# Optimization experiments

Measured on AMD Instinct MI355X. Metric: run time of the kernel, lower is better.

## Reference

```python
import jax, jax.numpy as jnp
import numpy as np

IMG_H = 448
IMG_W = 448
NEG = jnp.float32(-1e30)


def make_anchors(h, w, stride, size):
    # centers at (x*stride, y*stride), single scale, ratio 1; row-major (y, x) order
    ys = jnp.arange(h, dtype=jnp.float32) * stride
    xs = jnp.arange(w, dtype=jnp.float32) * stride
    cy, cx = jnp.meshgrid(ys, xs, indexing='ij')
    cx, cy = cx.reshape(-1), cy.reshape(-1)
    half = 0.5 * size
    return jnp.stack([cx - half, cy - half, cx + half, cy + half], axis=1)  # [h*w, 4]


def iou_one_vs_all(box, boxes):
    x1 = jnp.maximum(box[0], boxes[:, 0]); y1 = jnp.maximum(box[1], boxes[:, 1])
    x2 = jnp.minimum(box[2], boxes[:, 2]); y2 = jnp.minimum(box[3], boxes[:, 3])
    inter = jnp.maximum(x2 - x1, 0.) * jnp.maximum(y2 - y1, 0.)
    a1 = (box[2] - box[0]) * (box[3] - box[1])
    a2 = (boxes[:, 2] - boxes[:, 0]) * (boxes[:, 3] - boxes[:, 1])
    return inter / (a1 + a2 - inter)


def nms_topk(anchors, scores, valid, iou_thr, topk):
    # greedy NMS: invalid (<= mean) boxes get -inf score so they are never selected
    s0 = jnp.where(valid, scores, NEG)

    def body(k, carry):
        s, out = carry
        idx = jnp.argmax(s)
        box = anchors[idx]
        sup = iou_one_vs_all(box, anchors) > iou_thr
        s = jnp.where(sup, NEG, s).at[idx].set(NEG)
        out = out.at[k].set(box)
        return (s, out)

    _, out = jax.lax.fori_loop(0, topk, body, (s0, jnp.zeros((topk, 4), jnp.float32)))
    return out  # [topk, 4]


def get_att_roi(att, stride, size, iou_thr, topk):
    n, _, h, w = att.shape
    corner = jnp.zeros((h, w), att.dtype).at[int(0.1 * h):int(0.9 * h), int(0.1 * w):int(0.9 * w)].set(1.0)
    scores = (att[:, 0] * corner).reshape(n, -1)
    valid = scores > scores.mean(axis=1, keepdims=True)  # score threshold = per-sample mean
    anchors = make_anchors(h, w, float(stride), float(size))
    boxes = jax.vmap(lambda s, v: nms_topk(anchors, s, v, iou_thr, topk))(scores, valid)  # [n, topk, 4]
    boxes = jnp.stack([
        jnp.maximum(boxes[..., 0], 0.),
        jnp.maximum(boxes[..., 1], 0.),
        jnp.minimum(boxes[..., 2], IMG_W - 1.),
        jnp.minimum(boxes[..., 3], IMG_H - 1.),
    ], axis=-1)
    ids = jnp.broadcast_to(jnp.arange(n, dtype=jnp.float32)[:, None, None], (n, topk, 1))
    return jnp.concatenate([ids, boxes], axis=-1).reshape(n * topk, 5)


def crop_resize(xi, x1i, y1i, cw, ch):
    # bilinear resize of integer crop xi[:, y1i:y1i+ch, x1i:x1i+cw] to full (H, W),
    # align_corners=False (matches F.interpolate)
    C, H, W = xi.shape

    def axis_idx(n_out, start, clen):
        s = jnp.maximum((jnp.arange(n_out, dtype=jnp.float32) + 0.5) * (clen.astype(jnp.float32) / n_out) - 0.5, 0.)
        i0 = jnp.floor(s).astype(jnp.int32)
        i1 = jnp.minimum(i0 + 1, clen - 1)
        return start + i0, start + i1, s - i0

    gy0, gy1, fy = axis_idx(H, y1i, ch)
    gx0, gx1, fx = axis_idx(W, x1i, cw)
    x00 = xi[:, gy0[:, None], gx0[None, :]]
    x01 = xi[:, gy0[:, None], gx1[None, :]]
    x10 = xi[:, gy1[:, None], gx0[None, :]]
    x11 = xi[:, gy1[:, None], gx1[None, :]]
    top = x00 + fx[None, None, :] * (x01 - x00)
    bot = x10 + fx[None, None, :] * (x11 - x10)
    return top + fy[None, :, None] * (bot - top)


def forward(x2, x3, x4, x5):
    m3 = x3.mean(1, keepdims=True)
    m4 = x4.mean(1, keepdims=True)
    m5 = x5.mean(1, keepdims=True)
    roi3 = jax.lax.stop_gradient(get_att_roi(m3, 2 ** 3, 64, 0.05, 5))
    roi4 = jax.lax.stop_gradient(get_att_roi(m4, 2 ** 4, 128, 0.05, 3))
    roi5 = jax.lax.stop_gradient(get_att_roi(m5, 2 ** 5, 256, 0.05, 1))
    n = x2.shape[0]
    scale = float(2 ** 3)
    all_b = jnp.concatenate([
        roi3.reshape(n, 5, 5)[..., 1:],
        roi4.reshape(n, 3, 5)[..., 1:],
        roi5.reshape(n, 1, 5)[..., 1:],
    ], axis=1) / scale  # [n, 9, 4] in x2 feature coords
    x1i = jnp.floor(all_b[..., 0].min(1)).astype(jnp.int32)
    y1i = jnp.floor(all_b[..., 1].min(1)).astype(jnp.int32)
    x2i = jnp.floor(all_b[..., 2].max(1)).astype(jnp.int32)
    y2i = jnp.floor(all_b[..., 3].max(1)).astype(jnp.int32)
    crop = jax.vmap(crop_resize)(x2, x1i, y1i, x2i - x1i, y2i - y1i)
    return roi3, roi4, roi5, crop


def setup_inputs() -> dict:
    key = jax.random.key(0)
    k2, k3, k4, k5 = jax.random.split(key, 4)
    return {
        'x2': jax.random.normal(k2, (32, 256, 56, 56), jnp.float32),
        'x3': jax.random.normal(k3, (32, 256, 56, 56), jnp.float32),
        'x4': jax.random.normal(k4, (32, 256, 28, 28), jnp.float32),
        'x5': jax.random.normal(k5, (32, 256, 14, 14), jnp.float32),
    }


def reference(x2, x3, x4, x5):
    return forward(x2, x3, x4, x5)
```

## Files before the change

kernel.cpp:

```cpp
#include <hip/hip_runtime.h>

#define NEGV (-1e30f)

template <int H, int W, int R0, int R1>
__global__ __launch_bounds__(256) void mean_mask_kernel(const float* __restrict__ x,
                                                        float* __restrict__ scores) {
    constexpr int HW = H * W;
    constexpr int QUADS = HW / 4;
    const int tid = threadIdx.x;
    const int cg = tid >> 5;
    const int pl = tid & 31;
    const int q = blockIdx.x * 32 + pl;

    __shared__ float4 part[256];

    float4 acc = make_float4(0.f, 0.f, 0.f, 0.f);
    if (q < 32 * QUADS) {
        const int b = q / QUADS;
        const int quad = q - b * QUADS;
        const float* base = x + (size_t)b * 256 * HW + (size_t)cg * 32 * HW + quad * 4;
#pragma unroll 8
        for (int c = 0; c < 32; ++c) {
            const float4 v = *reinterpret_cast<const float4*>(base + (size_t)c * HW);
            acc.x += v.x; acc.y += v.y; acc.z += v.z; acc.w += v.w;
        }
    }
    part[tid] = acc;
    __syncthreads();

    if (tid < 32 && q < 32 * QUADS) {
        float4 s = part[pl];
#pragma unroll
        for (int g = 1; g < 8; ++g) {
            const float4 v = part[g * 32 + pl];
            s.x += v.x; s.y += v.y; s.z += v.z; s.w += v.w;
        }
        const int b = q / QUADS;
        const int quad = q - b * QUADS;
        const int p0 = quad * 4;
        float r[4] = {s.x, s.y, s.z, s.w};
        float o[4];
#pragma unroll
        for (int e = 0; e < 4; ++e) {
            const int p = p0 + e;
            const int y = p / W;
            const int xx = p - y * W;
            const float val = r[e] * (1.0f / 256.0f);
            const bool in = (y >= R0) && (y < R1) && (xx >= R0) && (xx < R1);
            o[e] = in ? val : 0.0f;
        }
        *reinterpret_cast<float4*>(scores + (size_t)b * HW + p0) =
            make_float4(o[0], o[1], o[2], o[3]);
    }
}

__global__ __launch_bounds__(256) void nms_kernel(const float* __restrict__ sc3,
                                                  const float* __restrict__ sc4,
                                                  const float* __restrict__ sc5,
                                                  float* __restrict__ out) {
    __shared__ float s[3136];
    __shared__ float red_v[256];
    __shared__ int red_i[256];

    const int blk = blockIdx.x;
    const int sid = blk >> 5;
    const int b = blk & 31;

    int HW, Wd, topk;
    float stride, size_;
    const float* sc;
    float* o;
    if (sid == 0) {
        HW = 3136; Wd = 56; topk = 5; stride = 8.f;  size_ = 64.f;
        sc = sc3 + (size_t)b * 3136; o = out + (size_t)(b * 5) * 5;
    } else if (sid == 1) {
        HW = 784;  Wd = 28; topk = 3; stride = 16.f; size_ = 128.f;
        sc = sc4 + (size_t)b * 784;  o = out + 800 + (size_t)(b * 3) * 5;
    } else {
        HW = 196;  Wd = 14; topk = 1; stride = 32.f; size_ = 256.f;
        sc = sc5 + (size_t)b * 196;  o = out + 1280 + (size_t)b * 5;
    }

    const int tid = threadIdx.x;

    float acc = 0.f;
    for (int j = tid; j < HW; j += 256) {
        const float v = sc[j];
        s[j] = v;
        acc += v;
    }
    red_v[tid] = acc;
    __syncthreads();
    for (int off = 128; off > 0; off >>= 1) {
        if (tid < off) red_v[tid] += red_v[tid + off];
        __syncthreads();
    }
    const float mean = red_v[0] / (float)HW;
    __syncthreads();

    for (int j = tid; j < HW; j += 256) {
        const float v = s[j];
        s[j] = (v > mean) ? v : NEGV;
    }
    __syncthreads();

    const float half = 0.5f * size_;
    const float area2 = 2.0f * size_ * size_;

    for (int k = 0; k < topk; ++k) {
        float bv = -3.0e38f;
        int bi = 0x7fffffff;
        for (int j = tid; j < HW; j += 256) {
            const float v = s[j];
            if (v > bv) { bv = v; bi = j; }
        }
        red_v[tid] = bv;
        red_i[tid] = bi;
        __syncthreads();
        for (int off = 128; off > 0; off >>= 1) {
            if (tid < off) {
                const float v2 = red_v[tid + off];
                const int i2 = red_i[tid + off];
                const float v1 = red_v[tid];
                const int i1 = red_i[tid];
                if (v2 > v1 || (v2 == v1 && i2 < i1)) {
                    red_v[tid] = v2;
                    red_i[tid] = i2;
                }
            }
            __syncthreads();
        }
        const int idx = red_i[0];

        const int gy = idx / Wd;
        const int gx = idx - gy * Wd;
        const float cx = (float)gx * stride;
        const float cy = (float)gy * stride;
        const float bx1 = cx - half, by1 = cy - half;
        const float bx2 = cx + half, by2 = cy + half;

        if (tid == 0) {
            float* r = o + (size_t)k * 5;
            r[0] = (float)b;
            r[1] = fmaxf(bx1, 0.f);
            r[2] = fmaxf(by1, 0.f);
            r[3] = fminf(bx2, 447.f);
            r[4] = fminf(by2, 447.f);
        }

        for (int j = tid; j < HW; j += 256) {
            const int ay = j / Wd;
            const int ax = j - ay * Wd;
            const float acx = (float)ax * stride;
            const float acy = (float)ay * stride;
            const float ix1 = fmaxf(bx1, acx - half);
            const float iy1 = fmaxf(by1, acy - half);
            const float ix2 = fminf(bx2, acx + half);
            const float iy2 = fminf(by2, acy + half);
            const float inter = fmaxf(ix2 - ix1, 0.f) * fmaxf(iy2 - iy1, 0.f);
            const float iou = inter / (area2 - inter);
            if (iou > 0.05f || j == idx) s[j] = NEGV;
        }
        __syncthreads();
    }
}

__global__ void bounds_kernel(const float* __restrict__ out, int* __restrict__ bnds) {
    const int b = threadIdx.x;
    if (b >= 32) return;
    float x1 = 3.0e38f, y1 = 3.0e38f, x2 = -3.0e38f, y2 = -3.0e38f;
#pragma unroll
    for (int k = 0; k < 5; ++k) {
        const float* r = out + (size_t)(b * 5 + k) * 5;
        x1 = fminf(x1, r[1]); y1 = fminf(y1, r[2]);
        x2 = fmaxf(x2, r[3]); y2 = fmaxf(y2, r[4]);
    }
#pragma unroll
    for (int k = 0; k < 3; ++k) {
        const float* r = out + 800 + (size_t)(b * 3 + k) * 5;
        x1 = fminf(x1, r[1]); y1 = fminf(y1, r[2]);
        x2 = fmaxf(x2, r[3]); y2 = fmaxf(y2, r[4]);
    }
    {
        const float* r = out + 1280 + (size_t)b * 5;
        x1 = fminf(x1, r[1]); y1 = fminf(y1, r[2]);
        x2 = fmaxf(x2, r[3]); y2 = fmaxf(y2, r[4]);
    }
    const int x1i = (int)floorf(x1 * 0.125f);
    const int y1i = (int)floorf(y1 * 0.125f);
    const int x2i = (int)floorf(x2 * 0.125f);
    const int y2i = (int)floorf(y2 * 0.125f);
    bnds[b * 4 + 0] = x1i;
    bnds[b * 4 + 1] = y1i;
    bnds[b * 4 + 2] = x2i - x1i;
    bnds[b * 4 + 3] = y2i - y1i;
}

__global__ __launch_bounds__(256) void crop_kernel(const float* __restrict__ x2,
                                                   const int* __restrict__ bnds,
                                                   float* __restrict__ out) {
    const int bc = blockIdx.x;
    const int b = bc >> 8;
    const int tid = threadIdx.x;

    const int x1i = bnds[b * 4 + 0];
    const int y1i = bnds[b * 4 + 1];
    const int cw = bnds[b * 4 + 2];
    const int ch = bnds[b * 4 + 3];
    const float sxs = (float)cw / 56.0f;
    const float sys = (float)ch / 56.0f;

    const float* plane = x2 + (size_t)bc * 3136;
    float* op = out + (size_t)bc * 3136;

    for (int p = tid; p < 3136; p += 256) {
        const int y = p / 56;
        const int xx = p - y * 56;
        const float sy = fmaxf((y + 0.5f) * sys - 0.5f, 0.f);
        const float sx = fmaxf((xx + 0.5f) * sxs - 0.5f, 0.f);
        const int iy0 = (int)sy;
        const int ix0 = (int)sx;
        const float fy = sy - (float)iy0;
        const float fx = sx - (float)ix0;
        const int iy1 = min(iy0 + 1, ch - 1);
        const int ix1 = min(ix0 + 1, cw - 1);
        const int gy0 = (y1i + iy0) * 56;
        const int gy1 = (y1i + iy1) * 56;
        const int gx0 = x1i + ix0;
        const int gx1 = x1i + ix1;
        const float v00 = plane[gy0 + gx0];
        const float v01 = plane[gy0 + gx1];
        const float v10 = plane[gy1 + gx0];
        const float v11 = plane[gy1 + gx1];
        const float top = v00 + fx * (v01 - v00);
        const float bot = v10 + fx * (v11 - v10);
        op[p] = top + fy * (bot - top);
    }
}

extern "C" void kernel_launch(void* const* d_in, const int* in_sizes, int n_in,
                              void* d_out, int out_size, void* d_ws, size_t ws_size,
                              hipStream_t stream) {
    const float* x2 = (const float*)d_in[0];
    const float* x3 = (const float*)d_in[1];
    const float* x4 = (const float*)d_in[2];
    const float* x5 = (const float*)d_in[3];
    float* out = (float*)d_out;

    float* sc3 = (float*)d_ws;
    float* sc4 = sc3 + 32 * 3136;
    float* sc5 = sc4 + 32 * 784;
    int* bnds = (int*)(sc5 + 32 * 196);

    mean_mask_kernel<56, 56, 5, 50><<<784, 256, 0, stream>>>(x3, sc3);
    mean_mask_kernel<28, 28, 2, 25><<<196, 256, 0, stream>>>(x4, sc4);
    mean_mask_kernel<14, 14, 1, 12><<<49, 256, 0, stream>>>(x5, sc5);

    nms_kernel<<<96, 256, 0, stream>>>(sc3, sc4, sc5, out);

    bounds_kernel<<<1, 64, 0, stream>>>(out, bnds);

    crop_kernel<<<8192, 256, 0, stream>>>(x2, bnds, out + 1440);
}
```

Baseline: 319.8 us.

## Fuse mean kernels, register-resident NMS, precomputed crop interpolation tables

```diff
diff --git a/kernel.cpp b/kernel.cpp
--- a/kernel.cpp
+++ b/kernel.cpp
@@ -3,40 +3,36 @@
 #define NEGV (-1e30f)
 
 template <int H, int W, int R0, int R1>
-__global__ __launch_bounds__(256) void mean_mask_kernel(const float* __restrict__ x,
-                                                        float* __restrict__ scores) {
+__device__ __forceinline__ void mean_body(int blk, const float* __restrict__ x,
+                                          float* __restrict__ scores,
+                                          float4* part) {
     constexpr int HW = H * W;
     constexpr int QUADS = HW / 4;
     const int tid = threadIdx.x;
     const int cg = tid >> 5;
     const int pl = tid & 31;
-    const int q = blockIdx.x * 32 + pl;
-
-    __shared__ float4 part[256];
+    const int q = blk * 32 + pl;
+
+    const int b = q / QUADS;
+    const int quad = q - b * QUADS;
+    const float* base = x + (size_t)b * 256 * HW + (size_t)cg * 32 * HW + quad * 4;
 
     float4 acc = make_float4(0.f, 0.f, 0.f, 0.f);
-    if (q < 32 * QUADS) {
-        const int b = q / QUADS;
-        const int quad = q - b * QUADS;
-        const float* base = x + (size_t)b * 256 * HW + (size_t)cg * 32 * HW + quad * 4;
 #pragma unroll 8
-        for (int c = 0; c < 32; ++c) {
-            const float4 v = *reinterpret_cast<const float4*>(base + (size_t)c * HW);
-            acc.x += v.x; acc.y += v.y; acc.z += v.z; acc.w += v.w;
-        }
+    for (int c = 0; c < 32; ++c) {
+        const float4 v = *reinterpret_cast<const float4*>(base + (size_t)c * HW);
+        acc.x += v.x; acc.y += v.y; acc.z += v.z; acc.w += v.w;
     }
     part[tid] = acc;
     __syncthreads();
 
-    if (tid < 32 && q < 32 * QUADS) {
+    if (tid < 32) {
         float4 s = part[pl];
 #pragma unroll
         for (int g = 1; g < 8; ++g) {
             const float4 v = part[g * 32 + pl];
             s.x += v.x; s.y += v.y; s.z += v.z; s.w += v.w;
         }
-        const int b = q / QUADS;
-        const int quad = q - b * QUADS;
         const int p0 = quad * 4;
         float r[4] = {s.x, s.y, s.z, s.w};
         float o[4];
@@ -54,93 +50,87 @@
     }
 }
 
-__global__ __launch_bounds__(256) void nms_kernel(const float* __restrict__ sc3,
-                                                  const float* __restrict__ sc4,
-                                                  const float* __restrict__ sc5,
-                                                  float* __restrict__ out) {
-    __shared__ float s[3136];
-    __shared__ float red_v[256];
-    __shared__ int red_i[256];
-
-    const int blk = blockIdx.x;
-    const int sid = blk >> 5;
-    const int b = blk & 31;
-
-    int HW, Wd, topk;
-    float stride, size_;
-    const float* sc;
-    float* o;
-    if (sid == 0) {
-        HW = 3136; Wd = 56; topk = 5; stride = 8.f;  size_ = 64.f;
-        sc = sc3 + (size_t)b * 3136; o = out + (size_t)(b * 5) * 5;
-    } else if (sid == 1) {
-        HW = 784;  Wd = 28; topk = 3; stride = 16.f; size_ = 128.f;
-        sc = sc4 + (size_t)b * 784;  o = out + 800 + (size_t)(b * 3) * 5;
+__global__ __launch_bounds__(256) void mean_all_kernel(const float* __restrict__ x3,
+                                                       const float* __restrict__ x4,
+                                                       const float* __restrict__ x5,
+                                                       float* __restrict__ sc3,
+                                                       float* __restrict__ sc4,
+                                                       float* __restrict__ sc5) {
+    __shared__ float4 part[256];
+    const int bid = blockIdx.x;
+    if (bid < 784) {
+        mean_body<56, 56, 5, 50>(bid, x3, sc3, part);
+    } else if (bid < 980) {
+        mean_body<28, 28, 2, 25>(bid - 784, x4, sc4, part);
     } else {
-        HW = 196;  Wd = 14; topk = 1; stride = 32.f; size_ = 256.f;
-        sc = sc5 + (size_t)b * 196;  o = out + 1280 + (size_t)b * 5;
-    }
-
+        mean_body<14, 14, 1, 12>(bid - 980, x5, sc5, part);
+    }
+}
+
+template <int HW, int W, int TOPK, int ISTRIDE, int ISIZE>
+__device__ __forceinline__ void nms_body(int b, const float* __restrict__ sc,
+                                         float* __restrict__ o,
+                                         float* rv, int* ri, float* rs) {
+    constexpr int NPT = (HW + 255) / 256;
     const int tid = threadIdx.x;
-
-    float acc = 0.f;
-    for (int j = tid; j < HW; j += 256) {
-        const float v = sc[j];
-        s[j] = v;
-        acc += v;
-    }
-    red_v[tid] = acc;
+    const int lane = tid & 63;
+    const int wave = tid >> 6;
+
+    float s[NPT];
+    float sum = 0.f;
+#pragma unroll
+    for (int i = 0; i < NPT; ++i) {
+        const int j = tid + 256 * i;
+        const float v = (j < HW) ? sc[j] : NEGV;
+        s[i] = v;
+        if (j < HW) sum += v;
+    }
+#pragma unroll
+    for (int off = 32; off > 0; off >>= 1) sum += __shfl_down(sum, off, 64);
+    if (lane == 0) rs[wave] = sum;
     __syncthreads();
-    for (int off = 128; off > 0; off >>= 1) {
-        if (tid < off) red_v[tid] += red_v[tid + off];
-        __syncthreads();
-    }
-    const float mean = red_v[0] / (float)HW;
-    __syncthreads();
-
-    for (int j = tid; j < HW; j += 256) {
-        const float v = s[j];
-        s[j] = (v > mean) ? v : NEGV;
-    }
-    __syncthreads();
-
-    const float half = 0.5f * size_;
-    const float area2 = 2.0f * size_ * size_;
-
-    for (int k = 0; k < topk; ++k) {
+    const float mean = (rs[0] + rs[1] + rs[2] + rs[3]) / (float)HW;
+
+#pragma unroll
+    for (int i = 0; i < NPT; ++i) s[i] = (s[i] > mean) ? s[i] : NEGV;
+
+    constexpr float half = 0.5f * (float)ISIZE;
+    constexpr float area2 = 2.0f * (float)ISIZE * (float)ISIZE;
+
+    for (int k = 0; k < TOPK; ++k) {
         float bv = -3.0e38f;
         int bi = 0x7fffffff;
-        for (int j = tid; j < HW; j += 256) {
-            const float v = s[j];
-            if (v > bv) { bv = v; bi = j; }
-        }
-        red_v[tid] = bv;
-        red_i[tid] = bi;
+#pragma unroll
+        for (int i = 0; i < NPT; ++i) {
+            if (s[i] > bv) { bv = s[i]; bi = tid + 256 * i; }
+        }
+#pragma unroll
+        for (int off = 32; off > 0; off >>= 1) {
+            const float ov = __shfl_down(bv, off, 64);
+            const int oi = __shfl_down(bi, off, 64);
+            if (ov > bv || (ov == bv && oi < bi)) { bv = ov; bi = oi; }
+        }
+        if (lane == 0) { rv[wave] = bv; ri[wave] = bi; }
         __syncthreads();
-        for (int off = 128; off > 0; off >>= 1) {
-            if (tid < off) {
-                const float v2 = red_v[tid + off];
-                const int i2 = red_i[tid + off];
-                const float v1 = red_v[tid];
-                const int i1 = red_i[tid];
-                if (v2 > v1 || (v2 == v1 && i2 < i1)) {
-                    red_v[tid] = v2;
-                    red_i[tid] = i2;
-                }
-            }
-            __syncthreads();
-        }
-        const int idx = red_i[0];
-
-        const int gy = idx / Wd;
-        const int gx = idx - gy * Wd;
-        const float cx = (float)gx * stride;
-        const float cy = (float)gy * stride;
-        const float bx1 = cx - half, by1 = cy - half;
-        const float bx2 = cx + half, by2 = cy + half;
+        float wv = rv[0];
+        int wi = ri[0];
+#pragma unroll
+        for (int w = 1; w < 4; ++w) {
+            const float v2 = rv[w];
+            const int i2 = ri[w];
+            if (v2 > wv || (v2 == wv && i2 < wi)) { wv = v2; wi = i2; }
+        }
+        __syncthreads();
+
+        const int gy = wi / W;
+        const int gx = wi - gy * W;
+        const float bx1 = (float)gx * (float)ISTRIDE - half;
+        const float by1 = (float)gy * (float)ISTRIDE - half;
+        const float bx2 = (float)gx * (float)ISTRIDE + half;
+        const float by2 = (float)gy * (float)ISTRIDE + half;
 
         if (tid == 0) {
-            float* r = o + (size_t)k * 5;
+            float* r = o + k * 5;
             r[0] = (float)b;
             r[1] = fmaxf(bx1, 0.f);
             r[2] = fmaxf(by1, 0.f);
@@ -148,93 +138,160 @@
             r[4] = fminf(by2, 447.f);
         }
 
-        for (int j = tid; j < HW; j += 256) {
-            const int ay = j / Wd;
-            const int ax = j - ay * Wd;
-            const float acx = (float)ax * stride;
-            const float acy = (float)ay * stride;
+#pragma unroll
+        for (int i = 0; i < NPT; ++i) {
+            const int j = tid + 256 * i;
+            const int ay = j / W;
+            const int ax = j - ay * W;
+            const float acx = (float)ax * (float)ISTRIDE;
+            const float acy = (float)ay * (float)ISTRIDE;
             const float ix1 = fmaxf(bx1, acx - half);
             const float iy1 = fmaxf(by1, acy - half);
             const float ix2 = fminf(bx2, acx + half);
             const float iy2 = fminf(by2, acy + half);
             const float inter = fmaxf(ix2 - ix1, 0.f) * fmaxf(iy2 - iy1, 0.f);
             const float iou = inter / (area2 - inter);
-            if (iou > 0.05f || j == idx) s[j] = NEGV;
-        }
-        __syncthreads();
-    }
-}
-
-__global__ void bounds_kernel(const float* __restrict__ out, int* __restrict__ bnds) {
-    const int b = threadIdx.x;
-    if (b >= 32) return;
-    float x1 = 3.0e38f, y1 = 3.0e38f, x2 = -3.0e38f, y2 = -3.0e38f;
-#pragma unroll
-    for (int k = 0; k < 5; ++k) {
-        const float* r = out + (size_t)(b * 5 + k) * 5;
-        x1 = fminf(x1, r[1]); y1 = fminf(y1, r[2]);
-        x2 = fmaxf(x2, r[3]); y2 = fmaxf(y2, r[4]);
-    }
-#pragma unroll
-    for (int k = 0; k < 3; ++k) {
-        const float* r = out + 800 + (size_t)(b * 3 + k) * 5;
-        x1 = fminf(x1, r[1]); y1 = fminf(y1, r[2]);
-        x2 = fmaxf(x2, r[3]); y2 = fmaxf(y2, r[4]);
-    }
-    {
-        const float* r = out + 1280 + (size_t)b * 5;
-        x1 = fminf(x1, r[1]); y1 = fminf(y1, r[2]);
-        x2 = fmaxf(x2, r[3]); y2 = fmaxf(y2, r[4]);
-    }
-    const int x1i = (int)floorf(x1 * 0.125f);
-    const int y1i = (int)floorf(y1 * 0.125f);
-    const int x2i = (int)floorf(x2 * 0.125f);
-    const int y2i = (int)floorf(y2 * 0.125f);
-    bnds[b * 4 + 0] = x1i;
-    bnds[b * 4 + 1] = y1i;
-    bnds[b * 4 + 2] = x2i - x1i;
-    bnds[b * 4 + 3] = y2i - y1i;
-}
-
-__global__ __launch_bounds__(256) void crop_kernel(const float* __restrict__ x2,
-                                                   const int* __restrict__ bnds,
-                                                   float* __restrict__ out) {
+            if (iou > 0.05f || j == wi) s[i] = NEGV;
+        }
+    }
+}
+
+__global__ __launch_bounds__(256) void nms_kernel(const float* __restrict__ sc3,
+                                                  const float* __restrict__ sc4,
+                                                  const float* __restrict__ sc5,
+                                                  float* __restrict__ out) {
+    __shared__ float rv[4];
+    __shared__ int ri[4];
+    __shared__ float rs[4];
+    const int blk = blockIdx.x;
+    const int sid = blk >> 5;
+    const int b = blk & 31;
+    if (sid == 0) {
+        nms_body<3136, 56, 5, 8, 64>(b, sc3 + (size_t)b * 3136, out + (size_t)b * 25, rv, ri, rs);
+    } else if (sid == 1) {
+        nms_body<784, 28, 3, 16, 128>(b, sc4 + (size_t)b * 784, out + 800 + (size_t)b * 15, rv, ri, rs);
+    } else {
+        nms_body<196, 14, 1, 32, 256>(b, sc5 + (size_t)b * 196, out + 1280 + (size_t)b * 5, rv, ri, rs);
+    }
+}
+
+__global__ __launch_bounds__(256) void tables_kernel(const float* __restrict__ out,
+                                                     int* __restrict__ ty0, int* __restrict__ ty1,
+                                                     float* __restrict__ tfy,
+                                                     int* __restrict__ tx0, int* __restrict__ tx1,
+                                                     float* __restrict__ tfx) {
+    __shared__ int sx1i[32], sy1i[32], scw[32], sch[32];
+    const int tid = threadIdx.x;
+    if (tid < 32) {
+        const int b = tid;
+        float x1 = 3.0e38f, y1 = 3.0e38f, x2 = -3.0e38f, y2 = -3.0e38f;
+#pragma unroll
+        for (int k = 0; k < 5; ++k) {
+            const float* r = out + (size_t)(b * 5 + k) * 5;
+            x1 = fminf(x1, r[1]); y1 = fminf(y1, r[2]);
+            x2 = fmaxf(x2, r[3]); y2 = fmaxf(y2, r[4]);
+        }
+#pragma unroll
+        for (int k = 0; k < 3; ++k) {
+            const float* r = out + 800 + (size_t)(b * 3 + k) * 5;
+            x1 = fminf(x1, r[1]); y1 = fminf(y1, r[2]);
+            x2 = fmaxf(x2, r[3]); y2 = fmaxf(y2, r[4]);
+        }
+        {
+            const float* r = out + 1280 + (size_t)b * 5;
+            x1 = fminf(x1, r[1]); y1 = fminf(y1, r[2]);
+            x2 = fmaxf(x2, r[3]); y2 = fmaxf(y2, r[4]);
+        }
+        const int x1i = (int)floorf(x1 * 0.125f);
+        const int y1i = (int)floorf(y1 * 0.125f);
+        const int x2i = (int)floorf(x2 * 0.125f);
+        const int y2i = (int)floorf(y2 * 0.125f);
+        sx1i[b] = x1i; sy1i[b] = y1i;
+        scw[b] = x2i - x1i; sch[b] = y2i - y1i;
+    }
+    __syncthreads();
+
+    for (int t = tid; t < 3584; t += 256) {
+        const int b = t / 112;
+        const int r = t - b * 112;
+        const int axis = r / 56;
+        const int o = r - axis * 56;
+        if (axis == 0) {
+            const int clen = sch[b];
+            const int start = sy1i[b];
+            const float s = fmaxf(((float)o + 0.5f) * ((float)clen / 56.0f) - 0.5f, 0.f);
+            const int i0 = (int)s;
+            const int i1 = min(i0 + 1, clen - 1);
+            ty0[b * 56 + o] = (start + i0) * 56;
+            ty1[b * 56 + o] = (start + i1) * 56;
+            tfy[b * 56 + o] = s - (float)i0;
+        } else {
+            const int clen = scw[b];
+            const int start = sx1i[b];
+            const float s = fmaxf(((float)o + 0.5f) * ((float)clen / 56.0f) - 0.5f, 0.f);
+            const int i0 = (int)s;
+            const int i1 = min(i0 + 1, clen - 1);
+            tx0[b * 56 + o] = start + i0;
+            tx1[b * 56 + o] = start + i1;
+            tfx[b * 56 + o] = s - (float)i0;
+        }
+    }
+}
+
+__global__ __launch_bounds__(448) void crop_kernel(const float* __restrict__ x2,
+                                                   const int* __restrict__ ty0,
+                                                   const int* __restrict__ ty1,
+                                                   const float* __restrict__ tfy,
+                                                   const int* __restrict__ tx0,
+                                                   const int* __restrict__ tx1,
+                                                   const float* __restrict__ tfx,
+                                                   float* __restrict__ outc) {
+    __shared__ int sy0[56], sy1[56];
+    __shared__ float sfy[56];
+    __shared__ int sx0[56], sx1[56];
+    __shared__ float sfx[56];
+
     const int bc = blockIdx.x;
     const int b = bc >> 8;
     const int tid = threadIdx.x;
 
-    const int x1i = bnds[b * 4 + 0];
-    const int y1i = bnds[b * 4 + 1];
-    const int cw = bnds[b * 4 + 2];
-    const int ch = bnds[b * 4 + 3];
-    const float sxs = (float)cw / 56.0f;
-    const float sys = (float)ch / 56.0f;
+    if (tid < 336) {
+        const int a = tid / 56;
+        const int o = tid - a * 56;
+        const int gi = b * 56 + o;
+        switch (a) {
+            case 0: sy0[o] = ty0[gi]; break;
+            case 1: sy1[o] = ty1[gi]; break;
+            case 2: sfy[o] = tfy[gi]; break;
+            case 3: sx0[o] = tx0[gi]; break;
+            case 4: sx1[o] = tx1[gi]; break;
+            default: sfx[o] = tfx[gi]; break;
+        }
+    }
+    __syncthreads();
+
+    const int y0 = tid / 56;
+    const int xx = tid - y0 * 56;
+    const int gx0 = sx0[xx];
+    const int gx1 = sx1[xx];
+    const float fx = sfx[xx];
 
     const float* plane = x2 + (size_t)bc * 3136;
-    float* op = out + (size_t)bc * 3136;
-
-    for (int p = tid; p < 3136; p += 256) {
-        const int y = p / 56;
-        const int xx = p - y * 56;
-        const float sy = fmaxf((y + 0.5f) * sys - 0.5f, 0.f);
-        const float sx = fmaxf((xx + 0.5f) * sxs - 0.5f, 0.f);
-        const int iy0 = (int)sy;
-        const int ix0 = (int)sx;
-        const float fy = sy - (float)iy0;
-        const float fx = sx - (float)ix0;
-        const int iy1 = min(iy0 + 1, ch - 1);
-        const int ix1 = min(ix0 + 1, cw - 1);
-        const int gy0 = (y1i + iy0) * 56;
-        const int gy1 = (y1i + iy1) * 56;
-        const int gx0 = x1i + ix0;
-        const int gx1 = x1i + ix1;
-        const float v00 = plane[gy0 + gx0];
-        const float v01 = plane[gy0 + gx1];
-        const float v10 = plane[gy1 + gx0];
-        const float v11 = plane[gy1 + gx1];
+    float* op = outc + (size_t)bc * 3136;
+
+#pragma unroll
+    for (int i = 0; i < 7; ++i) {
+        const int y = y0 + 8 * i;
+        const int r0 = sy0[y];
+        const int r1 = sy1[y];
+        const float fy = sfy[y];
+        const float v00 = plane[r0 + gx0];
+        const float v01 = plane[r0 + gx1];
+        const float v10 = plane[r1 + gx0];
+        const float v11 = plane[r1 + gx1];
         const float top = v00 + fx * (v01 - v00);
         const float bot = v10 + fx * (v11 - v10);
-        op[p] = top + fy * (bot - top);
+        op[tid + 448 * i] = top + fy * (bot - top);
     }
 }
 
@@ -250,15 +307,15 @@
     float* sc3 = (float*)d_ws;
     float* sc4 = sc3 + 32 * 3136;
     float* sc5 = sc4 + 32 * 784;
-    int* bnds = (int*)(sc5 + 32 * 196);
-
-    mean_mask_kernel<56, 56, 5, 50><<<784, 256, 0, stream>>>(x3, sc3);
-    mean_mask_kernel<28, 28, 2, 25><<<196, 256, 0, stream>>>(x4, sc4);
-    mean_mask_kernel<14, 14, 1, 12><<<49, 256, 0, stream>>>(x5, sc5);
-
+    int* ty0 = (int*)(sc5 + 32 * 196);
+    int* ty1 = ty0 + 32 * 56;
+    int* tx0 = ty1 + 32 * 56;
+    int* tx1 = tx0 + 32 * 56;
+    float* tfy = (float*)(tx1 + 32 * 56);
+    float* tfx = tfy + 32 * 56;
+
+    mean_all_kernel<<<1029, 256, 0, stream>>>(x3, x4, x5, sc3, sc4, sc5);
     nms_kernel<<<96, 256, 0, stream>>>(sc3, sc4, sc5, out);
-
-    bounds_kernel<<<1, 64, 0, stream>>>(out, bnds);
-
-    crop_kernel<<<8192, 256, 0, stream>>>(x2, bnds, out + 1440);
-}
+    tables_kernel<<<1, 256, 0, stream>>>(out, ty0, ty1, tfy, tx0, tx1, tfx);
+    crop_kernel<<<8192, 448, 0, stream>>>(x2, ty0, ty1, tfy, tx0, tx1, tfx, out + 1440);
+}
```

Result: faster. 291.7 us (-8.8%).
